# Kernel optimization log

Hardware: AMD Instinct MI355X
Metric: run time of the kernel (lower is better)

Reference implementation:

```python
import jax, jax.numpy as jnp
import numpy as np

DIM = 512
HEADS = 8
DIM_HEAD = 64
BLOCK_SIZE = 2048
B, N = 4, 2048
EPS = 1e-5


def setup_inputs() -> dict:
    key = jax.random.key(0)
    ks = jax.random.split(key, 8)
    hd = HEADS * DIM_HEAD
    std = 0.02
    return {
        "x": jax.random.normal(ks[0], (B, N, DIM), dtype=jnp.float32),
        "ln_w": jnp.ones((DIM,), jnp.float32),
        "ln_b": jnp.zeros((DIM,), jnp.float32),
        # linear weights stored [in, out]
        "wq": jax.random.normal(ks[1], (DIM, hd), jnp.float32) * std,
        "wk": jax.random.normal(ks[2], (DIM, hd), jnp.float32) * std,
        "wv": jax.random.normal(ks[3], (DIM, hd), jnp.float32) * std,
        "bv": jnp.zeros((hd,), jnp.float32),
        "wo": jax.random.normal(ks[4], (hd, DIM), jnp.float32) * std,
        "bo": jnp.zeros((DIM,), jnp.float32),
        "pe": jax.random.normal(ks[5], (1, BLOCK_SIZE, DIM), jnp.float32) * std,
    }


def reference(x, ln_w, ln_b, wq, wk, wv, bv, wo, bo, pe):
    # x: [b, n, dim] (channel_last=True path)
    b, n, _ = x.shape
    x_in = x
    # LayerNorm over last dim
    mu = jnp.mean(x, axis=-1, keepdims=True)
    var = jnp.var(x, axis=-1, keepdims=True)
    h = (x - mu) * jax.lax.rsqrt(var + EPS) * ln_w + ln_b
    # positional embedding
    h = h + pe[:, :n]
    # QKV projections -> [b, heads, n, dim_head]
    def split_heads(t):
        return t.reshape(b, n, HEADS, DIM_HEAD).transpose(0, 2, 1, 3)
    q = split_heads(h @ wq)
    k = split_heads(h @ wk)
    v = split_heads(h @ wv + bv)
    # attention
    scale = float(DIM_HEAD) ** -0.5
    attn = jnp.einsum('bhid,bhjd->bhij', q, k) * scale
    attn = jax.nn.softmax(attn, axis=-1)
    out = jnp.einsum('bhij,bhjd->bhid', attn, v)
    out = out.transpose(0, 2, 1, 3).reshape(b, n, HEADS * DIM_HEAD)
    out = out @ wo + bo
    return x_in + out
```

## Files before the change

kernel.cpp:

```cpp
#include <hip/hip_runtime.h>


typedef __bf16 bf16;
typedef __bf16 bf16x4 __attribute__((ext_vector_type(4)));
typedef __bf16 bf16x8 __attribute__((ext_vector_type(8)));
typedef float  f32x4  __attribute__((ext_vector_type(4)));
typedef float  f32x16 __attribute__((ext_vector_type(16)));
typedef unsigned int u32;
typedef u32 u32x4 __attribute__((ext_vector_type(4)));

#define MFMA16(a, b, c) __builtin_amdgcn_mfma_f32_16x16x32_bf16((a), (b), (c), 0, 0, 0)
#define MFMA32(a, b, c) __builtin_amdgcn_mfma_f32_32x32x16_bf16((a), (b), (c), 0, 0, 0)

#if __has_builtin(__builtin_amdgcn_exp2f)
#define EXP2(x) __builtin_amdgcn_exp2f(x)
#else
#define EXP2(x) exp2f(x)
#endif

__device__ __forceinline__ void gload16(const void* g, void* l) {
  __builtin_amdgcn_global_load_lds(
      (const __attribute__((address_space(1))) unsigned int*)g,
      (__attribute__((address_space(3))) unsigned int*)l, 16, 0, 0);
}

__device__ __forceinline__ u32 cvt_pk_bf16(float lo, float hi) {
  u32 r;
  asm("v_cvt_pk_bf16_f32 %0, %1, %2" : "=v"(r) : "v"(lo), "v"(hi));
  return r;
}
__device__ __forceinline__ void permswap(u32& a, u32& b) {
  asm volatile("v_permlane32_swap_b32 %0, %1" : "+v"(a), "+v"(b));
}

__global__ __launch_bounds__(256) void prep_kernel(
    const float* __restrict__ x, const float* __restrict__ lnw,
    const float* __restrict__ lnb, const float* __restrict__ pe,
    const float* __restrict__ wq, const float* __restrict__ wk,
    const float* __restrict__ wv, const float* __restrict__ wo,
    bf16* __restrict__ h, bf16* __restrict__ wqkvT, bf16* __restrict__ woT) {
  const int bid = blockIdx.x;
  if (bid < 1024) {
    __shared__ float tile[32][33];
    const int z = bid >> 8, r = bid & 255, bx = r >> 4, by = r & 15;
    const float* src = (z == 0) ? wq : (z == 1) ? wk : (z == 2) ? wv : wo;
    bf16* dst = (z < 3) ? (wqkvT + (size_t)z * 262144) : woT;
    const int tx = threadIdx.x & 31, ty = threadIdx.x >> 5;
#pragma unroll
    for (int yy = 0; yy < 4; ++yy)
      tile[ty + 8 * yy][tx] = src[(size_t)(by * 32 + ty + 8 * yy) * 512 + bx * 32 + tx];
    __syncthreads();
#pragma unroll
    for (int yy = 0; yy < 4; ++yy)
      dst[(size_t)(bx * 32 + ty + 8 * yy) * 512 + by * 32 + tx] =
          (bf16)tile[tx][ty + 8 * yy];
  } else {
    const int row = (bid - 1024) * 4 + (threadIdx.x >> 6);
    const int lane = threadIdx.x & 63;
    const float4* xr = (const float4*)(x + (size_t)row * 512) + lane * 2;
    const float4 a = xr[0], c = xr[1];
    float s = a.x + a.y + a.z + a.w + c.x + c.y + c.z + c.w;
    float ss = a.x * a.x + a.y * a.y + a.z * a.z + a.w * a.w +
               c.x * c.x + c.y * c.y + c.z * c.z + c.w * c.w;
#pragma unroll
    for (int off = 1; off <= 32; off <<= 1) {
      s += __shfl_xor(s, off);
      ss += __shfl_xor(ss, off);
    }
    const float mu = s * (1.0f / 512.0f);
    const float var = ss * (1.0f / 512.0f) - mu * mu;
    const float rs = rsqrtf(var + 1e-5f);
    const float4* wr = (const float4*)lnw + lane * 2;
    const float4* br = (const float4*)lnb + lane * 2;
    const float4* pr = (const float4*)(pe + (size_t)(row & 2047) * 512) + lane * 2;
    const float4 w0 = wr[0], w1 = wr[1], b0 = br[0], b1 = br[1], p0 = pr[0],
                 p1 = pr[1];
    bf16x8 o;
    o[0] = (bf16)((a.x - mu) * rs * w0.x + b0.x + p0.x);
    o[1] = (bf16)((a.y - mu) * rs * w0.y + b0.y + p0.y);
    o[2] = (bf16)((a.z - mu) * rs * w0.z + b0.z + p0.z);
    o[3] = (bf16)((a.w - mu) * rs * w0.w + b0.w + p0.w);
    o[4] = (bf16)((c.x - mu) * rs * w1.x + b1.x + p1.x);
    o[5] = (bf16)((c.y - mu) * rs * w1.y + b1.y + p1.y);
    o[6] = (bf16)((c.z - mu) * rs * w1.z + b1.z + p1.z);
    o[7] = (bf16)((c.w - mu) * rs * w1.w + b1.w + p1.w);
    *(bf16x8*)(h + (size_t)row * 512 + lane * 8) = o;
  }
}

template <int MI>
__device__ __forceinline__ void gemm_tile(const bf16* __restrict__ A,
                                          const bf16* __restrict__ Bt,
                                          f32x4 (&acc)[MI][4], char* lds) {
  constexpr int BM = MI * 32;
  constexpr int ABYTES = BM * 64;
  constexpr int BUFB = ABYTES + 8192;
  const int tid = threadIdx.x, wave = tid >> 6, lane = tid & 63;
  const int wrow = wave >> 1, wcol = wave & 1;
  const int l15 = lane & 15, lg = lane >> 4;
  const char* Ab = (const char*)A + (size_t)blockIdx.x * BM * 1024;
  const char* Bb = (const char*)Bt + (size_t)blockIdx.y * 128 * 1024;
  const int rA = wave * (BM / 4) + (lane >> 2);
  const int rB = wave * 32 + (lane >> 2);
  const int cb = (lane & 3) * 16;

  const f32x4 z = {0.f, 0.f, 0.f, 0.f};
#pragma unroll
  for (int mi = 0; mi < MI; ++mi)
#pragma unroll
    for (int ni = 0; ni < 4; ++ni) acc[mi][ni] = z;

#define GSTAGE(KT, NB)                                                         \
  {                                                                            \
    _Pragma("unroll") for (int i = 0; i < BM / 64; ++i)                        \
        gload16(Ab + (size_t)(rA + i * 16) * 1024 + cb + (KT)*64,              \
                (NB) + wave * (BM / 4) * 64 + i * 1024);                       \
    _Pragma("unroll") for (int i = 0; i < 2; ++i)                              \
        gload16(Bb + (size_t)(rB + i * 16) * 1024 + cb + (KT)*64,              \
                (NB) + ABYTES + wave * 2048 + i * 1024);                       \
  }

  GSTAGE(0, lds);
  __syncthreads();

  for (int kt = 0; kt < 16; ++kt) {
    if (kt < 15) GSTAGE(kt + 1, lds + ((kt + 1) & 1) * BUFB);
    char* lA = lds + (kt & 1) * BUFB;
    char* lB = lA + ABYTES;
    bf16x8 av[MI], bv[4];
#pragma unroll
    for (int mi = 0; mi < MI; ++mi)
      av[mi] = *(const bf16x8*)(lA + (wrow * (BM / 2) + mi * 16 + l15) * 64 + lg * 16);
#pragma unroll
    for (int ni = 0; ni < 4; ++ni)
      bv[ni] = *(const bf16x8*)(lB + (wcol * 64 + ni * 16 + l15) * 64 + lg * 16);
#pragma unroll
    for (int mi = 0; mi < MI; ++mi)
#pragma unroll
      for (int ni = 0; ni < 4; ++ni)
        acc[mi][ni] = MFMA16(av[mi], bv[ni], acc[mi][ni]);
    __syncthreads();
  }
#undef GSTAGE
}

__global__ __launch_bounds__(256, 3) void gemm_qkv_kernel(
    const bf16* __restrict__ h, const bf16* __restrict__ wqkvT,
    const float* __restrict__ bvec, bf16* __restrict__ qo, bf16* __restrict__ ko,
    bf16* __restrict__ vo) {
  __shared__ char lds[36864];
  f32x4 acc[4][4];
  gemm_tile<4>(h, wqkvT, acc, lds);
  const int tid = threadIdx.x, wave = tid >> 6, lane = tid & 63;
  const int wrow = wave >> 1, wcol = wave & 1;
  const int l15 = lane & 15, lg = lane >> 4;
  const int row0 = blockIdx.x * 128 + wrow * 64;
  const int col0 = blockIdx.y * 128 + wcol * 64;
  if (col0 >= 1024) {
    char* wl = lds + wave * 9216;
    const int hh = (col0 & 511) >> 6;
#pragma unroll
    for (int ni = 0; ni < 4; ++ni) {
      const float bias = bvec[(col0 & 511) + ni * 16 + l15];
      const int dl = ni * 16 + l15;
#pragma unroll
      for (int mi = 0; mi < 4; ++mi) {
        bf16x4 pv;
#pragma unroll
        for (int reg = 0; reg < 4; ++reg) pv[reg] = (bf16)(acc[mi][ni][reg] + bias);
        *(bf16x4*)(wl + dl * 144 + (mi * 16 + lg * 4) * 2) = pv;
      }
    }
    const int bb = row0 >> 11, n0 = row0 & 2047;
    bf16* vdst = vo + ((size_t)(bb * 8 + hh) * 64 + lane) * 2048 + n0;
#pragma unroll
    for (int i = 0; i < 8; ++i)
      *((uint4*)vdst + i) = *(uint4*)(wl + lane * 144 + i * 16);
  } else {
#pragma unroll
    for (int mi = 0; mi < 4; ++mi) {
#pragma unroll
      for (int ni = 0; ni < 4; ++ni) {
        int c = col0 + ni * 16 + l15;
        int proj = c >> 9;
        int wc = c & 511;
        int head = wc >> 6, d = wc & 63;
        int rb = row0 + mi * 16 + lg * 4;
        int bb = rb >> 11, n = rb & 2047;
        if (proj == 0) {
#pragma unroll
          for (int reg = 0; reg < 4; ++reg)
            qo[((size_t)(bb * 8 + head) * 2048 + (n + reg)) * 64 + d] =
                (bf16)(acc[mi][ni][reg] * (0.125f * 1.44269504f));
        } else {
#pragma unroll
          for (int reg = 0; reg < 4; ++reg)
            ko[((size_t)(bb * 8 + head) * 2048 + (n + reg)) * 64 + d] =
                (bf16)acc[mi][ni][reg];
        }
      }
    }
  }
}

__global__ __launch_bounds__(256, 2) void attn_kernel(const bf16* __restrict__ q,
                                                      const bf16* __restrict__ k,
                                                      const bf16* __restrict__ v,
                                                      bf16* __restrict__ ao) {
  __shared__ char lds[65536];
  const int tid = threadIdx.x, wave = tid >> 6, lane = tid & 63;
  const int l31 = lane & 31, hi = lane >> 5;

  const int bid = blockIdx.x;
  const int xcd = bid & 7, slot = bid >> 3;
  const int bh = xcd + 8 * (slot >> 4);
  const int qt = slot & 15;
  const int bb = bh >> 3, hh = bh & 7;

  const char* ksrc = (const char*)(k + (size_t)bh * 2048 * 64);
  const char* vsrc = (const char*)(v + (size_t)bh * 64 * 2048);

  const int krow0 = wave * 32 + (lane >> 3);
  const int kcolb = (lane & 7) * 16;
  const int vrow0 = wave * 16 + (lane >> 4);
  const int vcolb = (lane & 15) * 16;

  const int q0 = qt * 128 + wave * 32;
  const bf16* qbase = q + ((size_t)bh * 2048 + q0) * 64;
  bf16x8 qf[4];
#pragma unroll
  for (int ks = 0; ks < 4; ++ks)
    qf[ks] = *(const bf16x8*)(qbase + l31 * 64 + ks * 16 + hi * 8);

  f32x16 oacc[2] = {};
  float mrun = -1e30f, lrun = 0.f;

#define STAGE(T, BUF)                                                          \
  {                                                                            \
    char* Kd = (BUF);                                                          \
    char* Vd = (BUF) + 16384;                                                  \
    const char* kg = ksrc + (size_t)(T) * 16384;                               \
    const char* vg = vsrc + (size_t)(T) * 256;                                 \
    _Pragma("unroll") for (int i = 0; i < 4; ++i) {                            \
      int r = krow0 + i * 8;                                                   \
      gload16(kg + (size_t)r * 128 + (kcolb ^ ((r & 7) << 4)),                 \
              Kd + (wave * 32 + i * 8) * 128);                                 \
      int rv = vrow0 + i * 4;                                                  \
      gload16(vg + (size_t)rv * 4096 + (vcolb ^ ((rv & 15) << 4)),             \
              Vd + (wave * 16 + i * 4) * 256);                                 \
    }                                                                          \
  }

  STAGE(0, lds);
  __syncthreads();

  for (int t = 0; t < 16; ++t) {
    if (t + 1 < 16) STAGE(t + 1, lds + ((t + 1) & 1) * 32768);
    char* Ksh = lds + (t & 1) * 32768;
    char* Vsh = Ksh + 16384;

    f32x16 sacc[2][2];
#pragma unroll
    for (int sub = 0; sub < 2; ++sub) {
#pragma unroll
      for (int kt = 0; kt < 2; ++kt) {
        f32x16 sz = {};
        const int row = sub * 64 + kt * 32 + l31;
        const int swz = (row & 7) << 4;
#pragma unroll
        for (int ks = 0; ks < 4; ++ks) {
          bf16x8 kf = *(const bf16x8*)(Ksh + row * 128 + ((ks * 32 + hi * 16) ^ swz));
          sz = MFMA32(kf, qf[ks], sz);
        }
        sacc[sub][kt] = sz;
      }
    }

#pragma unroll
    for (int sub = 0; sub < 2; ++sub) {
      float mt = sacc[sub][0][0];
#pragma unroll
      for (int kt = 0; kt < 2; ++kt)
#pragma unroll
        for (int reg = 0; reg < 16; ++reg) mt = fmaxf(mt, sacc[sub][kt][reg]);
      mt = fmaxf(mt, __shfl_xor(mt, 32));
      if (__any(mt > mrun + 11.5f)) {
        float mn = fmaxf(mrun, mt);
        float sc = EXP2(mrun - mn);
        mrun = mn;
        lrun *= sc;
#pragma unroll
        for (int reg = 0; reg < 16; ++reg) {
          float s2 = __shfl(sc, (reg & 3) + 8 * (reg >> 2) + 4 * hi);
          oacc[0][reg] *= s2;
          oacc[1][reg] *= s2;
        }
      }
      float rs = 0.f;
      u32 c[2][8];
#pragma unroll
      for (int kt = 0; kt < 2; ++kt)
#pragma unroll
        for (int gp = 0; gp < 4; ++gp) {
          float p0 = EXP2(sacc[sub][kt][gp * 4 + 0] - mrun);
          float p1 = EXP2(sacc[sub][kt][gp * 4 + 1] - mrun);
          float p2 = EXP2(sacc[sub][kt][gp * 4 + 2] - mrun);
          float p3 = EXP2(sacc[sub][kt][gp * 4 + 3] - mrun);
          rs += (p0 + p1) + (p2 + p3);
          c[kt][gp * 2 + 0] = cvt_pk_bf16(p0, p1);
          c[kt][gp * 2 + 1] = cvt_pk_bf16(p2, p3);
        }
      lrun += rs;

      bf16x8 pf[4];
#pragma unroll
      for (int kt = 0; kt < 2; ++kt)
#pragma unroll
        for (int mm = 0; mm < 2; ++mm) {
          u32 a0 = c[kt][mm * 4 + 0], b0 = c[kt][mm * 4 + 2];
          u32 a1 = c[kt][mm * 4 + 1], b1 = c[kt][mm * 4 + 3];
          permswap(a0, b0);
          permswap(a1, b1);
          union { u32x4 w; bf16x8 v; } u;
          u.w = (u32x4){a0, a1, b0, b1};
          pf[kt * 2 + mm] = u.v;
        }

#pragma unroll
      for (int dt = 0; dt < 2; ++dt) {
        const int row = dt * 32 + l31;
        const int swz = (row & 15) << 4;
#pragma unroll
        for (int m = 0; m < 4; ++m) {
          bf16x8 vf = *(const bf16x8*)(Vsh + row * 256 +
                                       ((sub * 128 + m * 32 + hi * 16) ^ swz));
          oacc[dt] = MFMA32(pf[m], vf, oacc[dt]);
        }
      }
    }
    __syncthreads();
  }
#undef STAGE

  lrun += __shfl_xor(lrun, 32);
#if __has_builtin(__builtin_amdgcn_rcpf)
  float rin = __builtin_amdgcn_rcpf(lrun);
#else
  float rin = 1.0f / lrun;
#endif
#pragma unroll
  for (int reg = 0; reg < 16; ++reg) {
    int qrow = (reg & 3) + 8 * (reg >> 2) + 4 * hi;
    float rr = __shfl(rin, qrow);
    size_t base = ((size_t)bb * 2048 + q0 + qrow) * 512 + hh * 64;
    ao[base + l31] = (bf16)(oacc[0][reg] * rr);
    ao[base + 32 + l31] = (bf16)(oacc[1][reg] * rr);
  }
}

__global__ __launch_bounds__(256, 3) void gemm_out_kernel(
    const bf16* __restrict__ ao, const bf16* __restrict__ woT,
    const float* __restrict__ bo, const float* __restrict__ x,
    float* __restrict__ out) {
  __shared__ char lds[24576];
  f32x4 acc[2][4];
  gemm_tile<2>(ao, woT, acc, lds);
  const int tid = threadIdx.x, wave = tid >> 6, lane = tid & 63;
  const int wrow = wave >> 1, wcol = wave & 1;
  const int l15 = lane & 15, lg = lane >> 4;
  const int row0 = blockIdx.x * 64 + wrow * 32;
  const int col0 = blockIdx.y * 128 + wcol * 64;
#pragma unroll
  for (int mi = 0; mi < 2; ++mi) {
#pragma unroll
    for (int ni = 0; ni < 4; ++ni) {
      int c = col0 + ni * 16 + l15;
      float bias = bo[c];
#pragma unroll
      for (int reg = 0; reg < 4; ++reg) {
        int r = row0 + mi * 16 + lg * 4 + reg;
        size_t ofs = (size_t)r * 512 + c;
        out[ofs] = acc[mi][ni][reg] + bias + x[ofs];
      }
    }
  }
}

extern "C" void kernel_launch(void* const* d_in, const int* in_sizes, int n_in,
                              void* d_out, int out_size, void* d_ws, size_t ws_size,
                              hipStream_t stream) {
  const float* x   = (const float*)d_in[0];
  const float* lnw = (const float*)d_in[1];
  const float* lnb = (const float*)d_in[2];
  const float* wq  = (const float*)d_in[3];
  const float* wk  = (const float*)d_in[4];
  const float* wv  = (const float*)d_in[5];
  const float* bv  = (const float*)d_in[6];
  const float* wo  = (const float*)d_in[7];
  const float* bo  = (const float*)d_in[8];
  const float* pe  = (const float*)d_in[9];
  float* out = (float*)d_out;

  char* ws = (char*)d_ws;
  bf16* hbuf  = (bf16*)(ws);
  bf16* wqkvT = (bf16*)(ws + 8388608);
  bf16* woT   = (bf16*)(ws + 9961472);
  bf16* qb    = (bf16*)(ws + 10485760);
  bf16* kb    = (bf16*)(ws + 18874368);
  bf16* vb    = (bf16*)(ws + 27262976);
  bf16* aob   = hbuf;

  hipLaunchKernelGGL(prep_kernel, dim3(3072), dim3(256), 0, stream,
                     x, lnw, lnb, pe, wq, wk, wv, wo, hbuf, wqkvT, woT);
  hipLaunchKernelGGL(gemm_qkv_kernel, dim3(64, 12), dim3(256), 0, stream,
                     hbuf, wqkvT, bv, qb, kb, vb);
  hipLaunchKernelGGL(attn_kernel, dim3(512), dim3(256), 0, stream,
                     qb, kb, vb, aob);
  hipLaunchKernelGGL(gemm_out_kernel, dim3(128, 4), dim3(256), 0, stream,
                     aob, woT, bo, x, out);
}
```

Baseline: 173.7 us.

## Split attention KV range across wave pairs with smaller tiles and LDS merge

The attention kernel now assigns 64 query rows per block. Pairs of waves each process half of every 64-key tile, and the two partial softmax states are merged through LDS at the end. LDS per block is halved and launch bounds rise to 4 blocks per CU, with a grid of 1024 blocks, to raise occupancy and parallelism. s_setprio hints are also added around the MFMA sections. This costs a final LDS reduction and twice as many loop iterations with a barrier each, and K/V traffic per query grows because each block covers fewer queries.

```diff
diff --git a/kernel.cpp b/kernel.cpp
--- a/kernel.cpp
+++ b/kernel.cpp
@@ -203,29 +203,28 @@
   }
 }
 
-__global__ __launch_bounds__(256, 2) void attn_kernel(const bf16* __restrict__ q,
+__global__ __launch_bounds__(256, 4) void attn_kernel(const bf16* __restrict__ q,
                                                       const bf16* __restrict__ k,
                                                       const bf16* __restrict__ v,
                                                       bf16* __restrict__ ao) {
-  __shared__ char lds[65536];
+  __shared__ char lds[32768];
   const int tid = threadIdx.x, wave = tid >> 6, lane = tid & 63;
   const int l31 = lane & 31, hi = lane >> 5;
+  const int qsub = wave & 1, khalf = wave >> 1;
 
   const int bid = blockIdx.x;
   const int xcd = bid & 7, slot = bid >> 3;
-  const int bh = xcd + 8 * (slot >> 4);
-  const int qt = slot & 15;
+  const int bh = xcd + 8 * (slot >> 5);
+  const int qt = slot & 31;
   const int bb = bh >> 3, hh = bh & 7;
 
   const char* ksrc = (const char*)(k + (size_t)bh * 2048 * 64);
   const char* vsrc = (const char*)(v + (size_t)bh * 64 * 2048);
 
-  const int krow0 = wave * 32 + (lane >> 3);
-  const int kcolb = (lane & 7) * 16;
-  const int vrow0 = wave * 16 + (lane >> 4);
-  const int vcolb = (lane & 15) * 16;
-
-  const int q0 = qt * 128 + wave * 32;
+  const int srow = wave * 16 + (lane >> 3);
+  const int scol = (lane & 7) * 16;
+
+  const int q0 = qt * 64 + qsub * 32;
   const bf16* qbase = q + ((size_t)bh * 2048 + q0) * 64;
   bf16x8 qf[4];
 #pragma unroll
@@ -238,123 +237,134 @@
 #define STAGE(T, BUF)                                                          \
   {                                                                            \
     char* Kd = (BUF);                                                          \
-    char* Vd = (BUF) + 16384;                                                  \
-    const char* kg = ksrc + (size_t)(T) * 16384;                               \
-    const char* vg = vsrc + (size_t)(T) * 256;                                 \
-    _Pragma("unroll") for (int i = 0; i < 4; ++i) {                            \
-      int r = krow0 + i * 8;                                                   \
-      gload16(kg + (size_t)r * 128 + (kcolb ^ ((r & 7) << 4)),                 \
-              Kd + (wave * 32 + i * 8) * 128);                                 \
-      int rv = vrow0 + i * 4;                                                  \
-      gload16(vg + (size_t)rv * 4096 + (vcolb ^ ((rv & 15) << 4)),             \
-              Vd + (wave * 16 + i * 4) * 256);                                 \
+    char* Vd = (BUF) + 8192;                                                   \
+    const char* kg = ksrc + (size_t)(T)*8192;                                  \
+    const char* vg = vsrc + (size_t)(T)*128;                                   \
+    _Pragma("unroll") for (int i = 0; i < 2; ++i) {                            \
+      int r = srow + i * 8;                                                    \
+      int sw = scol ^ ((r & 7) << 4);                                          \
+      gload16(kg + (size_t)r * 128 + sw, Kd + (wave * 16 + i * 8) * 128);      \
+      gload16(vg + (size_t)r * 4096 + sw, Vd + (wave * 16 + i * 8) * 128);     \
     }                                                                          \
   }
 
   STAGE(0, lds);
   __syncthreads();
 
-  for (int t = 0; t < 16; ++t) {
-    if (t + 1 < 16) STAGE(t + 1, lds + ((t + 1) & 1) * 32768);
-    char* Ksh = lds + (t & 1) * 32768;
-    char* Vsh = Ksh + 16384;
-
-    f32x16 sacc[2][2];
-#pragma unroll
-    for (int sub = 0; sub < 2; ++sub) {
-#pragma unroll
-      for (int kt = 0; kt < 2; ++kt) {
-        f32x16 sz = {};
-        const int row = sub * 64 + kt * 32 + l31;
-        const int swz = (row & 7) << 4;
-#pragma unroll
-        for (int ks = 0; ks < 4; ++ks) {
-          bf16x8 kf = *(const bf16x8*)(Ksh + row * 128 + ((ks * 32 + hi * 16) ^ swz));
-          sz = MFMA32(kf, qf[ks], sz);
-        }
-        sacc[sub][kt] = sz;
-      }
-    }
-
-#pragma unroll
-    for (int sub = 0; sub < 2; ++sub) {
-      float mt = sacc[sub][0][0];
-#pragma unroll
-      for (int kt = 0; kt < 2; ++kt)
-#pragma unroll
-        for (int reg = 0; reg < 16; ++reg) mt = fmaxf(mt, sacc[sub][kt][reg]);
-      mt = fmaxf(mt, __shfl_xor(mt, 32));
-      if (__any(mt > mrun + 11.5f)) {
-        float mn = fmaxf(mrun, mt);
-        float sc = EXP2(mrun - mn);
-        mrun = mn;
-        lrun *= sc;
-#pragma unroll
-        for (int reg = 0; reg < 16; ++reg) {
-          float s2 = __shfl(sc, (reg & 3) + 8 * (reg >> 2) + 4 * hi);
-          oacc[0][reg] *= s2;
-          oacc[1][reg] *= s2;
-        }
-      }
-      float rs = 0.f;
-      u32 c[2][8];
-#pragma unroll
-      for (int kt = 0; kt < 2; ++kt)
-#pragma unroll
-        for (int gp = 0; gp < 4; ++gp) {
-          float p0 = EXP2(sacc[sub][kt][gp * 4 + 0] - mrun);
-          float p1 = EXP2(sacc[sub][kt][gp * 4 + 1] - mrun);
-          float p2 = EXP2(sacc[sub][kt][gp * 4 + 2] - mrun);
-          float p3 = EXP2(sacc[sub][kt][gp * 4 + 3] - mrun);
-          rs += (p0 + p1) + (p2 + p3);
-          c[kt][gp * 2 + 0] = cvt_pk_bf16(p0, p1);
-          c[kt][gp * 2 + 1] = cvt_pk_bf16(p2, p3);
-        }
-      lrun += rs;
-
-      bf16x8 pf[4];
-#pragma unroll
-      for (int kt = 0; kt < 2; ++kt)
-#pragma unroll
-        for (int mm = 0; mm < 2; ++mm) {
-          u32 a0 = c[kt][mm * 4 + 0], b0 = c[kt][mm * 4 + 2];
-          u32 a1 = c[kt][mm * 4 + 1], b1 = c[kt][mm * 4 + 3];
-          permswap(a0, b0);
-          permswap(a1, b1);
-          union { u32x4 w; bf16x8 v; } u;
-          u.w = (u32x4){a0, a1, b0, b1};
-          pf[kt * 2 + mm] = u.v;
-        }
-
-#pragma unroll
-      for (int dt = 0; dt < 2; ++dt) {
-        const int row = dt * 32 + l31;
-        const int swz = (row & 15) << 4;
-#pragma unroll
-        for (int m = 0; m < 4; ++m) {
-          bf16x8 vf = *(const bf16x8*)(Vsh + row * 256 +
-                                       ((sub * 128 + m * 32 + hi * 16) ^ swz));
-          oacc[dt] = MFMA32(pf[m], vf, oacc[dt]);
-        }
-      }
-    }
+  for (int t = 0; t < 32; ++t) {
+    if (t + 1 < 32) STAGE(t + 1, lds + ((t + 1) & 1) * 16384);
+    char* Ksh = lds + (t & 1) * 16384;
+    char* Vsh = Ksh + 8192;
+
+    f32x16 sacc = {};
+    {
+      const int row = khalf * 32 + l31;
+      const int swz = (row & 7) << 4;
+      __builtin_amdgcn_s_setprio(1);
+#pragma unroll
+      for (int ks = 0; ks < 4; ++ks) {
+        bf16x8 kf = *(const bf16x8*)(Ksh + row * 128 + ((ks * 32 + hi * 16) ^ swz));
+        sacc = MFMA32(kf, qf[ks], sacc);
+      }
+      __builtin_amdgcn_s_setprio(0);
+    }
+
+    float mt = sacc[0];
+#pragma unroll
+    for (int reg = 1; reg < 16; ++reg) mt = fmaxf(mt, sacc[reg]);
+    mt = fmaxf(mt, __shfl_xor(mt, 32));
+    if (__any(mt > mrun + 11.5f)) {
+      float mn = fmaxf(mrun, mt);
+      float sc = EXP2(mrun - mn);
+      mrun = mn;
+      lrun *= sc;
+#pragma unroll
+      for (int reg = 0; reg < 16; ++reg) {
+        float s2 = __shfl(sc, (reg & 3) + 8 * (reg >> 2) + 4 * hi);
+        oacc[0][reg] *= s2;
+        oacc[1][reg] *= s2;
+      }
+    }
+    float rs = 0.f;
+    u32 c[8];
+#pragma unroll
+    for (int gp = 0; gp < 8; ++gp) {
+      float p0 = EXP2(sacc[gp * 2 + 0] - mrun);
+      float p1 = EXP2(sacc[gp * 2 + 1] - mrun);
+      rs += p0 + p1;
+      c[gp] = cvt_pk_bf16(p0, p1);
+    }
+    lrun += rs;
+
+    bf16x8 pf[2];
+#pragma unroll
+    for (int kst = 0; kst < 2; ++kst) {
+      u32 a0 = c[kst * 4 + 0], a1 = c[kst * 4 + 1];
+      u32 b0 = c[kst * 4 + 2], b1 = c[kst * 4 + 3];
+      permswap(a0, b0);
+      permswap(a1, b1);
+      union { u32x4 w; bf16x8 v; } u;
+      u.w = (u32x4){a0, a1, b0, b1};
+      pf[kst] = u.v;
+    }
+
+    __builtin_amdgcn_s_setprio(1);
+#pragma unroll
+    for (int dt = 0; dt < 2; ++dt) {
+      const int row = dt * 32 + l31;
+      const int swz = (row & 7) << 4;
+#pragma unroll
+      for (int kst = 0; kst < 2; ++kst) {
+        bf16x8 vf = *(const bf16x8*)(
+            Vsh + row * 128 + ((khalf * 64 + kst * 32 + hi * 16) ^ swz));
+        oacc[dt] = MFMA32(pf[kst], vf, oacc[dt]);
+      }
+    }
+    __builtin_amdgcn_s_setprio(0);
     __syncthreads();
   }
 #undef STAGE
 
   lrun += __shfl_xor(lrun, 32);
+  char* mbase = lds + qsub * 8704;
+  if (khalf == 1) {
+#pragma unroll
+    for (int dt = 0; dt < 2; ++dt)
+#pragma unroll
+      for (int reg = 0; reg < 16; ++reg) {
+        int qrow = (reg & 3) + 8 * (reg >> 2) + 4 * hi;
+        *(float*)(mbase + (qrow * 64 + dt * 32 + l31) * 4) = oacc[dt][reg];
+      }
+    if (hi == 0) {
+      *(float*)(mbase + 8192 + l31 * 4) = mrun;
+      *(float*)(mbase + 8448 + l31 * 4) = lrun;
+    }
+  }
+  __syncthreads();
+  if (khalf == 0) {
+    float m1 = *(const float*)(mbase + 8192 + l31 * 4);
+    float l1 = *(const float*)(mbase + 8448 + l31 * 4);
+    float mM = fmaxf(mrun, m1);
+    float s0 = EXP2(mrun - mM), s1 = EXP2(m1 - mM);
+    float lt = lrun * s0 + l1 * s1;
 #if __has_builtin(__builtin_amdgcn_rcpf)
-  float rin = __builtin_amdgcn_rcpf(lrun);
+    float rin = __builtin_amdgcn_rcpf(lt);
 #else
-  float rin = 1.0f / lrun;
+    float rin = 1.0f / lt;
 #endif
-#pragma unroll
-  for (int reg = 0; reg < 16; ++reg) {
-    int qrow = (reg & 3) + 8 * (reg >> 2) + 4 * hi;
-    float rr = __shfl(rin, qrow);
-    size_t base = ((size_t)bb * 2048 + q0 + qrow) * 512 + hh * 64;
-    ao[base + l31] = (bf16)(oacc[0][reg] * rr);
-    ao[base + 32 + l31] = (bf16)(oacc[1][reg] * rr);
+    float a0 = s0 * rin, a1 = s1 * rin;
+#pragma unroll
+    for (int dt = 0; dt < 2; ++dt)
+#pragma unroll
+      for (int reg = 0; reg < 16; ++reg) {
+        int qrow = (reg & 3) + 8 * (reg >> 2) + 4 * hi;
+        float w0 = __shfl(a0, qrow);
+        float w1 = __shfl(a1, qrow);
+        float o1 = *(const float*)(mbase + (qrow * 64 + dt * 32 + l31) * 4);
+        float val = oacc[dt][reg] * w0 + o1 * w1;
+        ao[((size_t)bb * 2048 + q0 + qrow) * 512 + hh * 64 + dt * 32 + l31] =
+            (bf16)val;
+      }
   }
 }
 
@@ -414,7 +424,7 @@
                      x, lnw, lnb, pe, wq, wk, wv, wo, hbuf, wqkvT, woT);
   hipLaunchKernelGGL(gemm_qkv_kernel, dim3(64, 12), dim3(256), 0, stream,
                      hbuf, wqkvT, bv, qb, kb, vb);
-  hipLaunchKernelGGL(attn_kernel, dim3(512), dim3(256), 0, stream,
+  hipLaunchKernelGGL(attn_kernel, dim3(1024), dim3(256), 0, stream,
                      qb, kb, vb, aob);
   hipLaunchKernelGGL(gemm_out_kernel, dim3(128, 4), dim3(256), 0, stream,
                      aob, woT, bo, x, out);
```

Result: no change. 172.0 us (-1.0%).
